# Optimization experiments

Hardware: AMD Instinct MI355X
Metric: run time of the kernel (lower is better)

The kernel has to match this reference:

```python
import jax, jax.numpy as jnp
import numpy as np

BINS = 6
THRESH = 0.2
OUT_HW = (240, 240)


def _normalize(x, lo=0.0, hi=1.0):
    # torch: if max-min==0 return zeros, else affine rescale to [lo, hi]
    mn, mx = x.min(), x.max()
    rng = mx - mn
    safe = jnp.where(rng == 0, 1.0, rng)
    out = (x - mn) / safe * (hi - lo) + lo
    return jnp.where(rng == 0, jnp.zeros_like(x), out)


def _ponder(x):
    w = (x.max() - x.mean()) ** 2
    return _normalize(x) * w


def _zero_border(x):
    # zero first/last row and column (works batched over leading dims)
    return (x.at[..., 0, :].set(0.0)
             .at[..., :, 0].set(0.0)
             .at[..., -1, :].set(0.0)
             .at[..., :, -1].set(0.0))


def _rarity(ch):
    # ch: [H, W] single feature channel
    ch = _zero_border(ch)
    ch = _normalize(ch, 0.0, 256.0)
    # torch.histc(bins=BINS, min=0, max=256): last bin includes the max value
    bin_idx = jnp.clip(jnp.floor(ch / (256.0 / BINS)), 0, BINS - 1).astype(jnp.int32)
    hist = jnp.zeros((BINS,), ch.dtype).at[bin_idx].add(1.0)
    hist = -jnp.log(hist / hist.sum() + 0.0001)
    # (channel * bins - 1).long().clamp(0, bins-1): .long() truncates toward zero
    gidx = jnp.clip(jnp.trunc(ch * BINS - 1.0), 0, BINS - 1).astype(jnp.int32)
    dst = _normalize(hist[gidx], 0.0, 1.0)
    return _ponder(dst)


def _apply_rarity(layer):
    # layer: [1, C, H, W] -> per-channel rarity, ponderated sum, threshold
    ch = layer[0]  # [C, H, W]
    r = jax.vmap(_rarity)(ch)  # [C, H, W]
    rz = _zero_border(r)
    # channel 0 keeps its border (torch code only zeroes borders for i >= 1)
    maps = jnp.concatenate([r[:1], rz[1:]], axis=0)
    proc = jax.vmap(_ponder)(maps).sum(0)
    proc = _normalize(proc, 0.0, 1.0)
    return jnp.where(proc < THRESH, 0.0, proc)


def _group(layer):
    resized = jax.image.resize(_apply_rarity(layer), OUT_HW, 'bilinear')
    # pack of one layer: fuse_itti == map_ponderation of the single map
    return _normalize(_ponder(resized), 0.0, 256.0)


def _forward(l1, l2, l3, l4, l5):
    groups = jnp.stack([_group(l) for l in (l1, l2, l3, l4, l5)], axis=-1)  # [240,240,5]
    return groups.sum(-1), groups


def setup_inputs() -> dict:
    key = jax.random.key(0)
    ks = jax.random.split(key, 5)
    shapes = [(1, 64, 480, 480), (1, 128, 240, 240), (1, 256, 120, 120),
              (1, 512, 60, 60), (1, 512, 30, 30)]
    return {f"l{i+1}": jax.random.uniform(ks[i], shapes[i], jnp.float32)
            for i in range(5)}


def reference(l1, l2, l3, l4, l5):
    return _forward(l1, l2, l3, l4, l5)
```

## Files before the change

### kernel.cpp

```cpp
#include <hip/hip_runtime.h>
#include <math.h>

#define TPB 256

constexpr int DIMS_[5]  = {480, 240, 120, 60, 30};
constexpr int CHS_ [5]  = {64, 128, 256, 512, 512};
constexpr int CHB_ [5]  = {0, 64, 192, 448, 960};
constexpr int TOTCH     = 1472;
constexpr int PROCB_[5] = {0, 230400, 288000, 302400, 306000};
constexpr int PROCTOT   = 306900;

constexpr int O_CHMIN = 0;
constexpr int O_CHMAX = 1472;
constexpr int O_HIST  = 2944;
constexpr int O_GCNT  = 11776;
constexpr int O_CLUT  = 20608;
constexpr int O_BSUM  = O_CLUT + 16 * 1472;
constexpr int O_PMIN  = O_BSUM + 5;
constexpr int O_PMAX  = O_PMIN + 5;
constexpr int O_S3MIN = O_PMAX + 5;
constexpr int O_S3MAX = O_S3MIN + 5;
constexpr int O_S3SUM = O_S3MAX + 5;
constexpr int O_PROC  = 44192;
constexpr int O_RESZ  = O_PROC + PROCTOT;
constexpr int N_INIT  = O_PROC + PROCTOT;

struct P {
  const float* in[5];
  float* ws;
};

__device__ __forceinline__ void mk_hthr(float mn, float rng, float* th) {
  if (rng == 0.0f) { th[0]=th[1]=th[2]=th[3]=th[4]=INFINITY; return; }
  th[0] = mn + rng * (1.0f / 6.0f); th[1] = mn + rng * (2.0f / 6.0f);
  th[2] = mn + rng * (3.0f / 6.0f); th[3] = mn + rng * (4.0f / 6.0f);
  th[4] = mn + rng * (5.0f / 6.0f);
}
__device__ __forceinline__ void mk_gthr(float mn, float rng, float* tg) {
  if (rng == 0.0f) { tg[0]=tg[1]=tg[2]=tg[3]=tg[4]=INFINITY; return; }
  tg[0] = mn + rng * (2.0f / 1536.0f); tg[1] = mn + rng * (3.0f / 1536.0f);
  tg[2] = mn + rng * (4.0f / 1536.0f); tg[3] = mn + rng * (5.0f / 1536.0f);
  tg[4] = mn + rng * (6.0f / 1536.0f);
}

__global__ void k_init(float* ws) {
  int i = blockIdx.x * TPB + threadIdx.x;
  if (i >= N_INIT) return;
  unsigned v = 0u;
  if (i < O_CHMAX) v = 0x7F800000u;
  else if (i >= O_PMIN  && i < O_PMAX)  v = 0x7F800000u;
  else if (i >= O_S3MIN && i < O_S3MAX) v = 0x7F800000u;
  ((unsigned*)ws)[i] = v;
}

template <int L>
__device__ void bodyA(int local, const float* __restrict__ in, float* ws) {
  constexpr int D = DIMS_[L], HW = D * D, HW4 = HW / 4;
  constexpr int BPC = (HW4 + 4095) / 4096;
  constexpr int DQ = D / 4;
  int ch = local / BPC, chunk = local % BPC;
  int nvec = HW4 - chunk * 4096; if (nvec > 4096) nvec = 4096;
  const float4* pv = (const float4*)(in + (size_t)ch * HW) + (size_t)chunk * 4096;
  int t = threadIdx.x;
  float mn = INFINITY, mx = 0.0f;
  #pragma unroll 4
  for (int i = 0; i < 16; i++) {
    int vi = i * TPB + t;
    if (vi < nvec) {
      float4 v = pv[vi];
      float vv[4] = {v.x, v.y, v.z, v.w};
      int f4i = chunk * 4096 + vi;
      if constexpr (D % 4 == 0) {
        int y = f4i / DQ, xq = f4i - y * DQ;
        if (y == 0 || y == D - 1) { vv[0] = vv[1] = vv[2] = vv[3] = 0.0f; }
        else {
          if (xq == 0)      vv[0] = 0.0f;
          if (xq == DQ - 1) vv[3] = 0.0f;
        }
      } else {
        int e0 = f4i * 4;
        #pragma unroll
        for (int j = 0; j < 4; j++) {
          int e = e0 + j, y = e / D, x = e - y * D;
          bool inr = ((unsigned)(x - 1) < (unsigned)(D - 2)) && ((unsigned)(y - 1) < (unsigned)(D - 2));
          if (!inr) vv[j] = 0.0f;
        }
      }
      #pragma unroll
      for (int j = 0; j < 4; j++) { mn = fminf(mn, vv[j]); mx = fmaxf(mx, vv[j]); }
    }
  }
  for (int o = 32; o; o >>= 1) { mn = fminf(mn, __shfl_down(mn, o)); mx = fmaxf(mx, __shfl_down(mx, o)); }
  __shared__ float smn[4], smx[4];
  int w = t >> 6;
  if ((t & 63) == 0) { smn[w] = mn; smx[w] = mx; }
  __syncthreads();
  if (t == 0) {
    mn = fminf(fminf(smn[0], smn[1]), fminf(smn[2], smn[3]));
    mx = fmaxf(fmaxf(smx[0], smx[1]), fmaxf(smx[2], smx[3]));
    int g = CHB_[L] + ch;
    atomicMin((unsigned*)ws + O_CHMIN + g, __float_as_uint(mn));
    atomicMax((unsigned*)ws + O_CHMAX + g, __float_as_uint(mx));
  }
}
__global__ void kA(P p) {
  int b = blockIdx.x;
  if      (b <  960) bodyA<0>(b,        p.in[0], p.ws);
  else if (b < 1472) bodyA<1>(b -  960, p.in[1], p.ws);
  else if (b < 1728) bodyA<2>(b - 1472, p.in[2], p.ws);
  else if (b < 2240) bodyA<3>(b - 1728, p.in[3], p.ws);
  else               bodyA<4>(b - 2240, p.in[4], p.ws);
}

template <int L>
__device__ void bodyB(int local, const float* __restrict__ in, float* ws) {
  constexpr int D = DIMS_[L], HW = D * D, HW4 = HW / 4;
  constexpr int BPC = (HW4 + 4095) / 4096;
  constexpr int DQ = D / 4;
  int ch = local / BPC, chunk = local % BPC;
  int g = CHB_[L] + ch;
  float mn = ws[O_CHMIN + g], mx = ws[O_CHMAX + g], rng = mx - mn;
  float th[5], tg[5];
  mk_hthr(mn, rng, th);
  mk_gthr(mn, rng, tg);
  int nvec = HW4 - chunk * 4096; if (nvec > 4096) nvec = 4096;
  const float4* pv = (const float4*)(in + (size_t)ch * HW) + (size_t)chunk * 4096;
  int t = threadIdx.x;
  unsigned c[10] = {0u,0u,0u,0u,0u,0u,0u,0u,0u,0u};
  unsigned nval = 0u;
  #pragma unroll 4
  for (int i = 0; i < 16; i++) {
    int vi = i * TPB + t;
    if (vi < nvec) {
      float4 v = pv[vi];
      float vv[4] = {v.x, v.y, v.z, v.w};
      int f4i = chunk * 4096 + vi;
      if constexpr (D % 4 == 0) {
        int y = f4i / DQ, xq = f4i - y * DQ;
        if (y == 0 || y == D - 1) { vv[0] = vv[1] = vv[2] = vv[3] = 0.0f; }
        else {
          if (xq == 0)      vv[0] = 0.0f;
          if (xq == DQ - 1) vv[3] = 0.0f;
        }
      } else {
        int e0 = f4i * 4;
        #pragma unroll
        for (int j = 0; j < 4; j++) {
          int e = e0 + j, y = e / D, x = e - y * D;
          bool inr = ((unsigned)(x - 1) < (unsigned)(D - 2)) && ((unsigned)(y - 1) < (unsigned)(D - 2));
          if (!inr) vv[j] = 0.0f;
        }
      }
      nval += 4u;
      #pragma unroll
      for (int j = 0; j < 4; j++) {
        float x = vv[j];
        #pragma unroll
        for (int k = 0; k < 5; k++) {
          c[k]     += (x >= th[k]);
          c[5 + k] += (x >= tg[k]);
        }
      }
    }
  }
  #pragma unroll
  for (int k = 0; k < 10; k++)
    for (int o = 32; o; o >>= 1) c[k] += __shfl_down(c[k], o);
  for (int o = 32; o; o >>= 1) nval += __shfl_down(nval, o);
  if ((t & 63) == 0) {
    unsigned* H = (unsigned*)ws + O_HIST + g * 6;
    unsigned* G = (unsigned*)ws + O_GCNT + g * 6;
    atomicAdd(H + 0, nval - c[0]); atomicAdd(H + 1, c[0] - c[1]);
    atomicAdd(H + 2, c[1] - c[2]); atomicAdd(H + 3, c[2] - c[3]);
    atomicAdd(H + 4, c[3] - c[4]); atomicAdd(H + 5, c[4]);
    atomicAdd(G + 0, nval - c[5]); atomicAdd(G + 1, c[5] - c[6]);
    atomicAdd(G + 2, c[6] - c[7]); atomicAdd(G + 3, c[7] - c[8]);
    atomicAdd(G + 4, c[8] - c[9]); atomicAdd(G + 5, c[9]);
  }
}
__global__ void kB(P p) {
  int b = blockIdx.x;
  if      (b <  960) bodyB<0>(b,        p.in[0], p.ws);
  else if (b < 1472) bodyB<1>(b -  960, p.in[1], p.ws);
  else if (b < 1728) bodyB<2>(b - 1472, p.in[2], p.ws);
  else if (b < 2240) bodyB<3>(b - 1728, p.in[3], p.ws);
  else               bodyB<4>(b - 2240, p.in[4], p.ws);
}

__global__ void kS(P p) {
  int ch = blockIdx.x * TPB + threadIdx.x;
  if (ch >= TOTCH) return;
  float* ws = p.ws;
  int l = (ch < 64) ? 0 : (ch < 192) ? 1 : (ch < 448) ? 2 : (ch < 960) ? 3 : 4;
  int D = DIMS_[l];
  int HW = D * D;
  int c0 = ch - CHB_[l];
  unsigned hc[6], gc[6];
  unsigned* H = (unsigned*)ws + O_HIST + ch * 6;
  unsigned* G = (unsigned*)ws + O_GCNT + ch * 6;
  #pragma unroll
  for (int k = 0; k < 6; k++) { hc[k] = H[k]; gc[k] = G[k]; }
  float HWf = (float)HW;
  float nh[6];
  #pragma unroll
  for (int k = 0; k < 6; k++) nh[k] = -logf((float)hc[k] / HWf + 1e-4f);
  float dmn = INFINITY, dmx = -INFINITY;
  #pragma unroll
  for (int k = 0; k < 6; k++) if (gc[k]) { dmn = fminf(dmn, nh[k]); dmx = fmaxf(dmx, nh[k]); }
  float dr = dmx - dmn;
  float dstn[6];
  #pragma unroll
  for (int k = 0; k < 6; k++) dstn[k] = (dr == 0.0f) ? 0.0f : ((nh[k] - dmn) / dr);
  float maxv = (dr == 0.0f) ? 0.0f : 1.0f;
  double s1 = 0.0;
  #pragma unroll
  for (int k = 0; k < 6; k++) s1 += (double)gc[k] * (double)dstn[k];
  float mean1 = (float)(s1 / (double)HW);
  float w1 = maxv - mean1; w1 *= w1;
  float lut1[6];
  #pragma unroll
  for (int k = 0; k < 6; k++) lut1[k] = dstn[k] * w1;
  float mnc = ws[O_CHMIN + ch], mxc = ws[O_CHMAX + ch];
  float tg[5];
  mk_gthr(mnc, mxc - mnc, tg);
  int gb = (0.0f >= tg[0]) + (0.0f >= tg[1]) + (0.0f >= tg[2]) + (0.0f >= tg[3]) + (0.0f >= tg[4]);
  unsigned bcnt = (unsigned)(4 * D - 4);
  float lmn, lmx;
  double s2 = 0.0;
  if (c0 == 0) {
    lmn = INFINITY; lmx = -INFINITY;
    #pragma unroll
    for (int k = 0; k < 6; k++) if (gc[k]) {
      lmn = fminf(lmn, lut1[k]); lmx = fmaxf(lmx, lut1[k]);
      s2 += (double)gc[k] * (double)lut1[k];
    }
  } else {
    lmn = 0.0f; lmx = 0.0f;
    #pragma unroll
    for (int k = 0; k < 6; k++) {
      unsigned ic = gc[k] - ((k == gb) ? bcnt : 0u);
      if (ic) {
        lmn = fminf(lmn, lut1[k]); lmx = fmaxf(lmx, lut1[k]);
        s2 += (double)ic * (double)lut1[k];
      }
    }
  }
  float mean2 = (float)(s2 / (double)HW);
  float w2 = lmx - mean2; w2 *= w2;
  float r2 = lmx - lmn;
  float lout[6];
  #pragma unroll
  for (int k = 0; k < 6; k++) lout[k] = (r2 == 0.0f) ? 0.0f : (((lut1[k] - lmn) / r2) * w2);
  float* T = ws + O_CLUT + (size_t)ch * 16;
  #pragma unroll
  for (int k = 0; k < 5; k++) T[5 + k] = tg[k];
  #pragma unroll
  for (int k = 0; k < 6; k++) T[10 + k] = lout[k];
  float bc = (c0 == 0) ? lout[gb] : ((r2 == 0.0f) ? 0.0f : (((0.0f - lmn) / r2) * w2));
  atomicAdd(ws + O_BSUM + l, bc);
}

template <int L>
__device__ void bodyC(int local, const float* __restrict__ in, float* ws,
                      float* slut, float* sred) {
  constexpr int D = DIMS_[L], HW = D * D, HW4 = HW / 4, C = CHS_[L];
  constexpr int NT  = (HW4 + 63) / 64;
  constexpr int NCH = C / 64;
  int tile = local % NT, chunk = local / NT;
  int cbase = CHB_[L] + chunk * 64;
  int t = threadIdx.x, lane = t & 63, w = t >> 6;
  const float* gl = ws + O_CLUT + (size_t)cbase * 16;
  for (int i = t; i < 1024; i += TPB) slut[i] = gl[i];
  __syncthreads();
  int p4 = tile * 64 + lane;
  bool valid = p4 < HW4;
  float a0 = 0.0f, a1 = 0.0f, a2 = 0.0f, a3 = 0.0f;
  if (valid) {
    const float4* bp = (const float4*)in + (size_t)(chunk * 64 + w * 16) * HW4 + p4;
    const float* su = slut + (w * 16) * 16;
    #pragma unroll 4
    for (int c = 0; c < 16; c++) {
      float4 v = bp[(size_t)c * HW4];
      const float* cl = su + c * 16 + 5;
      float g0 = cl[0], g1 = cl[1], g2 = cl[2], g3 = cl[3], g4 = cl[4];
      float l0 = cl[5], l1 = cl[6], l2 = cl[7], l3 = cl[8], l4 = cl[9], l5 = cl[10];
      float s;
      s = (v.x >= g0) ? l1 : l0; s = (v.x >= g1) ? l2 : s; s = (v.x >= g2) ? l3 : s;
      s = (v.x >= g3) ? l4 : s;  s = (v.x >= g4) ? l5 : s; a0 += s;
      s = (v.y >= g0) ? l1 : l0; s = (v.y >= g1) ? l2 : s; s = (v.y >= g2) ? l3 : s;
      s = (v.y >= g3) ? l4 : s;  s = (v.y >= g4) ? l5 : s; a1 += s;
      s = (v.z >= g0) ? l1 : l0; s = (v.z >= g1) ? l2 : s; s = (v.z >= g2) ? l3 : s;
      s = (v.z >= g3) ? l4 : s;  s = (v.z >= g4) ? l5 : s; a2 += s;
      s = (v.w >= g0) ? l1 : l0; s = (v.w >= g1) ? l2 : s; s = (v.w >= g2) ? l3 : s;
      s = (v.w >= g3) ? l4 : s;  s = (v.w >= g4) ? l5 : s; a3 += s;
    }
  }
  sred[0 * 256 + w * 64 + lane] = a0;
  sred[1 * 256 + w * 64 + lane] = a1;
  sred[2 * 256 + w * 64 + lane] = a2;
  sred[3 * 256 + w * 64 + lane] = a3;
  __syncthreads();
  if (w == 0 && valid) {
    float o[4];
    #pragma unroll
    for (int j = 0; j < 4; j++)
      o[j] = sred[j * 256 + lane] + sred[j * 256 + 64 + lane] +
             sred[j * 256 + 128 + lane] + sred[j * 256 + 192 + lane];
    float bs = ws[O_BSUM + L];
    float* procL = ws + O_PROC + PROCB_[L];
    int px0 = p4 * 4;
    if constexpr (NCH == 1) {
      #pragma unroll
      for (int j = 0; j < 4; j++) {
        int px = px0 + j, y = px / D, x = px - y * D;
        bool inr = ((unsigned)(x - 1) < (unsigned)(D - 2)) && ((unsigned)(y - 1) < (unsigned)(D - 2));
        if (!inr) o[j] = bs;
      }
      ((float4*)procL)[p4] = make_float4(o[0], o[1], o[2], o[3]);
    } else {
      #pragma unroll
      for (int j = 0; j < 4; j++) {
        int px = px0 + j, y = px / D, x = px - y * D;
        bool inr = ((unsigned)(x - 1) < (unsigned)(D - 2)) && ((unsigned)(y - 1) < (unsigned)(D - 2));
        if (inr) atomicAdd(procL + px, o[j]);
        else if (chunk == 0) procL[px] = bs;
      }
    }
  }
}
__global__ __launch_bounds__(TPB) void kC(P p) {
  __shared__ float slut[1024];
  __shared__ float sred[1024];
  int b = blockIdx.x;
  if      (b <  900) bodyC<0>(b,        p.in[0], p.ws, slut, sred);
  else if (b < 1350) bodyC<1>(b -  900, p.in[1], p.ws, slut, sred);
  else if (b < 1578) bodyC<2>(b - 1350, p.in[2], p.ws, slut, sred);
  else if (b < 1698) bodyC<3>(b - 1578, p.in[3], p.ws, slut, sred);
  else               bodyC<4>(b - 1698, p.in[4], p.ws, slut, sred);
}

template <int L>
__device__ void bodyD(int chunk, float* ws) {
  constexpr int HW = DIMS_[L] * DIMS_[L];
  const float* pr = ws + O_PROC + PROCB_[L];
  int t = threadIdx.x;
  float mn = INFINITY, mx = 0.0f;
  #pragma unroll
  for (int i = 0; i < 16; i++) {
    int idx = chunk * 4096 + i * TPB + t;
    if (idx < HW) { float v = pr[idx]; mn = fminf(mn, v); mx = fmaxf(mx, v); }
  }
  for (int o = 32; o; o >>= 1) { mn = fminf(mn, __shfl_down(mn, o)); mx = fmaxf(mx, __shfl_down(mx, o)); }
  __shared__ float smn[4], smx[4];
  int w = t >> 6;
  if ((t & 63) == 0) { smn[w] = mn; smx[w] = mx; }
  __syncthreads();
  if (t == 0) {
    mn = fminf(fminf(smn[0], smn[1]), fminf(smn[2], smn[3]));
    mx = fmaxf(fmaxf(smx[0], smx[1]), fmaxf(smx[2], smx[3]));
    atomicMin((unsigned*)ws + O_PMIN + L, __float_as_uint(mn));
    atomicMax((unsigned*)ws + O_PMAX + L, __float_as_uint(mx));
  }
}
__global__ void kD(P p) {
  int b = blockIdx.x;
  if      (b < 57) bodyD<0>(b,      p.ws);
  else if (b < 72) bodyD<1>(b - 57, p.ws);
  else if (b < 76) bodyD<2>(b - 72, p.ws);
  else if (b < 77) bodyD<3>(b - 76, p.ws);
  else             bodyD<4>(b - 77, p.ws);
}

template <int L>
__device__ float bodyF(int px, float* ws) {
  constexpr int D = DIMS_[L];
  constexpr float INV = (float)D / 240.0f;
  constexpr float KS = (INV > 1.0f) ? INV : 1.0f;
  int oy = px / 240, ox = px - oy * 240;
  float mnv = __uint_as_float(((unsigned*)ws)[O_PMIN + L]);
  float mxv = __uint_as_float(((unsigned*)ws)[O_PMAX + L]);
  float pr = mxv - mnv;
  const float* procL = ws + O_PROC + PROCB_[L];
  float sfy = ((float)oy + 0.5f) * INV - 0.5f;
  float sfx = ((float)ox + 0.5f) * INV - 0.5f;
  int y0 = (int)ceilf(sfy - KS);  if (y0 < 0) y0 = 0;
  int y1 = (int)floorf(sfy + KS); if (y1 > D - 1) y1 = D - 1;
  int x0 = (int)ceilf(sfx - KS);  if (x0 < 0) x0 = 0;
  int x1 = (int)floorf(sfx + KS); if (x1 > D - 1) x1 = D - 1;
  float wsx = 0.0f;
  for (int jx = x0; jx <= x1; jx++) wsx += fmaxf(1.0f - fabsf(sfx - (float)jx) / KS, 0.0f);
  float acc = 0.0f, wsy = 0.0f;
  for (int jy = y0; jy <= y1; jy++) {
    float wy = fmaxf(1.0f - fabsf(sfy - (float)jy) / KS, 0.0f);
    wsy += wy;
    if (wy > 0.0f) {
      const float* row = procL + jy * D;
      float rs = 0.0f;
      for (int jx = x0; jx <= x1; jx++) {
        float wx = fmaxf(1.0f - fabsf(sfx - (float)jx) / KS, 0.0f);
        if (wx > 0.0f) {
          float v = row[jx];
          float tv = (pr == 0.0f) ? 0.0f : ((v - mnv) / pr);
          tv = (tv < 0.2f) ? 0.0f : tv;
          rs += wx * tv;
        }
      }
      acc += wy * rs;
    }
  }
  return acc / (wsy * wsx);
}
__global__ void kF(P p) {
  float* ws = p.ws;
  int b = blockIdx.x, l = b / 225;
  int px = (b - l * 225) * TPB + threadIdx.x;
  float res;
  switch (l) {
    case 0: res = bodyF<0>(px, ws); break;
    case 1: res = bodyF<1>(px, ws); break;
    case 2: res = bodyF<2>(px, ws); break;
    case 3: res = bodyF<3>(px, ws); break;
    default: res = bodyF<4>(px, ws); break;
  }
  ws[O_RESZ + l * 57600 + px] = res;
  float mn = res, mx = res, s = res;
  for (int o = 32; o; o >>= 1) {
    mn = fminf(mn, __shfl_down(mn, o));
    mx = fmaxf(mx, __shfl_down(mx, o));
    s += __shfl_down(s, o);
  }
  __shared__ float smn[4], smx[4], ssm[4];
  int t = threadIdx.x, w = t >> 6;
  if ((t & 63) == 0) { smn[w] = mn; smx[w] = mx; ssm[w] = s; }
  __syncthreads();
  if (t == 0) {
    mn = fminf(fminf(smn[0], smn[1]), fminf(smn[2], smn[3]));
    mx = fmaxf(fmaxf(smx[0], smx[1]), fmaxf(smx[2], smx[3]));
    s = ssm[0] + ssm[1] + ssm[2] + ssm[3];
    atomicMin((unsigned*)ws + O_S3MIN + l, __float_as_uint(mn));
    atomicMax((unsigned*)ws + O_S3MAX + l, __float_as_uint(mx));
    atomicAdd(ws + O_S3SUM + l, s);
  }
}

__global__ void kG2(P p, float* __restrict__ out) {
  float* ws = p.ws;
  int px = blockIdx.x * TPB + threadIdx.x;
  float sum = 0.0f;
  #pragma unroll
  for (int l = 0; l < 5; l++) {
    float v = ws[O_RESZ + l * 57600 + px];
    float mn3 = __uint_as_float(((unsigned*)ws)[O_S3MIN + l]);
    float mx3 = __uint_as_float(((unsigned*)ws)[O_S3MAX + l]);
    float mean3 = ws[O_S3SUM + l] / 57600.0f;
    float r3 = mx3 - mn3;
    float ov;
    if (r3 == 0.0f) ov = 0.0f;
    else {
      float w3 = mx3 - mean3; w3 *= w3;
      if (w3 == 0.0f) ov = 0.0f;
      else ov = ((v - mn3) / r3) * w3 / w3 * 256.0f;
    }
    out[57600 + px * 5 + l] = ov;
    sum += ov;
  }
  out[px] = sum;
}

extern "C" void kernel_launch(void* const* d_in, const int* in_sizes, int n_in,
                              void* d_out, int out_size, void* d_ws, size_t ws_size,
                              hipStream_t stream) {
  (void)in_sizes; (void)n_in; (void)out_size; (void)ws_size;
  P p;
  for (int i = 0; i < 5; i++) p.in[i] = (const float*)d_in[i];
  p.ws = (float*)d_ws;
  float* out = (float*)d_out;

  k_init<<<(N_INIT + TPB - 1) / TPB, TPB, 0, stream>>>(p.ws);
  kA  <<<2752, TPB, 0, stream>>>(p);
  kB  <<<2752, TPB, 0, stream>>>(p);
  kS  <<<6,    TPB, 0, stream>>>(p);
  kC  <<<1730, TPB, 0, stream>>>(p);
  kD  <<<78,   TPB, 0, stream>>>(p);
  kF  <<<1125, TPB, 0, stream>>>(p);
  kG2 <<<225,  TPB, 0, stream>>>(p, out);
}
```

Before: 288.6 us.

## Software-pipeline loads in reduction kernels and move border masking out of histogram pass

The min/max, histogram and LUT-accumulate loops now use explicit double-buffered float4 loads in groups of four, so the next group's global loads are issued before the current group is processed. The histogram pass no longer zeroes border pixels per element. Extra blocks instead subtract the border pixels' raw counts, and the summary kernel adds back the border count as zeros. Per-thread nval tracking is dropped and the LUT layout in workspace is reindexed. This trades extra blocks, atomics and register pressure for less index arithmetic and better latency hiding in the bandwidth-bound passes.

```diff
diff --git a/kernel.cpp b/kernel.cpp
--- a/kernel.cpp
+++ b/kernel.cpp
@@ -53,6 +53,16 @@
   ((unsigned*)ws)[i] = v;
 }
 
+template <int D, int DQ>
+__device__ __forceinline__ void zb4(int f4i, float4& v) {
+  int y = f4i / DQ, xq = f4i - y * DQ;
+  if (y == 0 || y == D - 1) { v.x = v.y = v.z = v.w = 0.0f; }
+  else {
+    if (xq == 0)      v.x = 0.0f;
+    if (xq == DQ - 1) v.w = 0.0f;
+  }
+}
+
 template <int L>
 __device__ void bodyA(int local, const float* __restrict__ in, float* ws) {
   constexpr int D = DIMS_[L], HW = D * D, HW4 = HW / 4;
@@ -63,31 +73,56 @@
   const float4* pv = (const float4*)(in + (size_t)ch * HW) + (size_t)chunk * 4096;
   int t = threadIdx.x;
   float mn = INFINITY, mx = 0.0f;
-  #pragma unroll 4
-  for (int i = 0; i < 16; i++) {
-    int vi = i * TPB + t;
-    if (vi < nvec) {
-      float4 v = pv[vi];
-      float vv[4] = {v.x, v.y, v.z, v.w};
-      int f4i = chunk * 4096 + vi;
-      if constexpr (D % 4 == 0) {
-        int y = f4i / DQ, xq = f4i - y * DQ;
-        if (y == 0 || y == D - 1) { vv[0] = vv[1] = vv[2] = vv[3] = 0.0f; }
-        else {
-          if (xq == 0)      vv[0] = 0.0f;
-          if (xq == DQ - 1) vv[3] = 0.0f;
+  auto MM4 = [&](float4 v) {
+    mn = fminf(fminf(mn, fminf(v.x, v.y)), fminf(v.z, v.w));
+    mx = fmaxf(fmaxf(mx, fmaxf(v.x, v.y)), fmaxf(v.z, v.w));
+  };
+  if constexpr (D % 4 == 0) {
+    if (nvec == 4096) {
+      int base = chunk * 4096;
+      float4 a0 = pv[t], a1 = pv[t + TPB], a2 = pv[t + 2 * TPB], a3 = pv[t + 3 * TPB];
+      #pragma unroll
+      for (int g = 0; g < 4; g++) {
+        float4 b0 = a0, b1 = a1, b2 = a2, b3 = a3;
+        if (g < 3) {
+          int o = (g + 1) * 4 * TPB + t;
+          b0 = pv[o]; b1 = pv[o + TPB]; b2 = pv[o + 2 * TPB]; b3 = pv[o + 3 * TPB];
         }
-      } else {
-        int e0 = f4i * 4;
+        int i0 = base + g * 4 * TPB + t;
+        zb4<D, DQ>(i0,           a0); MM4(a0);
+        zb4<D, DQ>(i0 + TPB,     a1); MM4(a1);
+        zb4<D, DQ>(i0 + 2 * TPB, a2); MM4(a2);
+        zb4<D, DQ>(i0 + 3 * TPB, a3); MM4(a3);
+        a0 = b0; a1 = b1; a2 = b2; a3 = b3;
+      }
+    } else {
+      #pragma unroll 4
+      for (int i = 0; i < 16; i++) {
+        int vi = i * TPB + t;
+        if (vi < nvec) {
+          float4 v = pv[vi];
+          zb4<D, DQ>(chunk * 4096 + vi, v);
+          MM4(v);
+        }
+      }
+    }
+  } else {
+    #pragma unroll 4
+    for (int i = 0; i < 16; i++) {
+      int vi = i * TPB + t;
+      if (vi < nvec) {
+        float4 v = pv[vi];
+        float vv[4] = {v.x, v.y, v.z, v.w};
+        int e0 = (chunk * 4096 + vi) * 4;
         #pragma unroll
         for (int j = 0; j < 4; j++) {
           int e = e0 + j, y = e / D, x = e - y * D;
           bool inr = ((unsigned)(x - 1) < (unsigned)(D - 2)) && ((unsigned)(y - 1) < (unsigned)(D - 2));
           if (!inr) vv[j] = 0.0f;
         }
-      }
-      #pragma unroll
-      for (int j = 0; j < 4; j++) { mn = fminf(mn, vv[j]); mx = fmaxf(mx, vv[j]); }
+        v.x = vv[0]; v.y = vv[1]; v.z = vv[2]; v.w = vv[3];
+        MM4(v);
+      }
     }
   }
   for (int o = 32; o; o >>= 1) { mn = fminf(mn, __shfl_down(mn, o)); mx = fmaxf(mx, __shfl_down(mx, o)); }
@@ -116,7 +151,6 @@
 __device__ void bodyB(int local, const float* __restrict__ in, float* ws) {
   constexpr int D = DIMS_[L], HW = D * D, HW4 = HW / 4;
   constexpr int BPC = (HW4 + 4095) / 4096;
-  constexpr int DQ = D / 4;
   int ch = local / BPC, chunk = local % BPC;
   int g = CHB_[L] + ch;
   float mn = ws[O_CHMIN + g], mx = ws[O_CHMAX + g], rng = mx - mn;
@@ -127,59 +161,79 @@
   const float4* pv = (const float4*)(in + (size_t)ch * HW) + (size_t)chunk * 4096;
   int t = threadIdx.x;
   unsigned c[10] = {0u,0u,0u,0u,0u,0u,0u,0u,0u,0u};
-  unsigned nval = 0u;
-  #pragma unroll 4
-  for (int i = 0; i < 16; i++) {
-    int vi = i * TPB + t;
-    if (vi < nvec) {
-      float4 v = pv[vi];
-      float vv[4] = {v.x, v.y, v.z, v.w};
-      int f4i = chunk * 4096 + vi;
-      if constexpr (D % 4 == 0) {
-        int y = f4i / DQ, xq = f4i - y * DQ;
-        if (y == 0 || y == D - 1) { vv[0] = vv[1] = vv[2] = vv[3] = 0.0f; }
-        else {
-          if (xq == 0)      vv[0] = 0.0f;
-          if (xq == DQ - 1) vv[3] = 0.0f;
-        }
-      } else {
-        int e0 = f4i * 4;
-        #pragma unroll
-        for (int j = 0; j < 4; j++) {
-          int e = e0 + j, y = e / D, x = e - y * D;
-          bool inr = ((unsigned)(x - 1) < (unsigned)(D - 2)) && ((unsigned)(y - 1) < (unsigned)(D - 2));
-          if (!inr) vv[j] = 0.0f;
-        }
-      }
-      nval += 4u;
-      #pragma unroll
-      for (int j = 0; j < 4; j++) {
-        float x = vv[j];
-        #pragma unroll
-        for (int k = 0; k < 5; k++) {
-          c[k]     += (x >= th[k]);
-          c[5 + k] += (x >= tg[k]);
-        }
-      }
+  auto CNT = [&](float x) {
+    #pragma unroll
+    for (int k = 0; k < 5; k++) { c[k] += (x >= th[k]); c[5 + k] += (x >= tg[k]); }
+  };
+  auto CNT4 = [&](float4 v) { CNT(v.x); CNT(v.y); CNT(v.z); CNT(v.w); };
+  if (nvec == 4096) {
+    float4 a0 = pv[t], a1 = pv[t + TPB], a2 = pv[t + 2 * TPB], a3 = pv[t + 3 * TPB];
+    #pragma unroll
+    for (int gq = 0; gq < 4; gq++) {
+      float4 b0 = a0, b1 = a1, b2 = a2, b3 = a3;
+      if (gq < 3) {
+        int o = (gq + 1) * 4 * TPB + t;
+        b0 = pv[o]; b1 = pv[o + TPB]; b2 = pv[o + 2 * TPB]; b3 = pv[o + 3 * TPB];
+      }
+      CNT4(a0); CNT4(a1); CNT4(a2); CNT4(a3);
+      a0 = b0; a1 = b1; a2 = b2; a3 = b3;
+    }
+  } else {
+    #pragma unroll 4
+    for (int i = 0; i < 16; i++) {
+      int vi = i * TPB + t;
+      if (vi < nvec) CNT4(pv[vi]);
     }
   }
   #pragma unroll
   for (int k = 0; k < 10; k++)
     for (int o = 32; o; o >>= 1) c[k] += __shfl_down(c[k], o);
-  for (int o = 32; o; o >>= 1) nval += __shfl_down(nval, o);
   if ((t & 63) == 0) {
     unsigned* H = (unsigned*)ws + O_HIST + g * 6;
     unsigned* G = (unsigned*)ws + O_GCNT + g * 6;
-    atomicAdd(H + 0, nval - c[0]); atomicAdd(H + 1, c[0] - c[1]);
-    atomicAdd(H + 2, c[1] - c[2]); atomicAdd(H + 3, c[2] - c[3]);
-    atomicAdd(H + 4, c[3] - c[4]); atomicAdd(H + 5, c[4]);
-    atomicAdd(G + 0, nval - c[5]); atomicAdd(G + 1, c[5] - c[6]);
-    atomicAdd(G + 2, c[6] - c[7]); atomicAdd(G + 3, c[7] - c[8]);
-    atomicAdd(G + 4, c[8] - c[9]); atomicAdd(G + 5, c[9]);
-  }
-}
+    #pragma unroll
+    for (int k = 0; k < 5; k++) { atomicAdd(H + k, c[k]); atomicAdd(G + k, c[5 + k]); }
+  }
+}
+
+__device__ void bodyBborder(int ch, P p) {
+  float* ws = p.ws;
+  int l = (ch < 64) ? 0 : (ch < 192) ? 1 : (ch < 448) ? 2 : (ch < 960) ? 3 : 4;
+  int D = DIMS_[l];
+  const float* src = p.in[l] + (size_t)(ch - CHB_[l]) * (D * D);
+  float mn = ws[O_CHMIN + ch], mx = ws[O_CHMAX + ch], rng = mx - mn;
+  float th[5], tg[5];
+  mk_hthr(mn, rng, th);
+  mk_gthr(mn, rng, tg);
+  unsigned c[10] = {0u,0u,0u,0u,0u,0u,0u,0u,0u,0u};
+  int nb = 4 * D - 4;
+  for (int e = threadIdx.x; e < nb; e += TPB) {
+    int x, y;
+    if (e < D)          { y = 0; x = e; }
+    else if (e < 2 * D) { y = D - 1; x = e - D; }
+    else {
+      int e2 = e - 2 * D;
+      y = 1 + (e2 >> 1);
+      x = (e2 & 1) ? (D - 1) : 0;
+    }
+    float v = src[y * D + x];
+    #pragma unroll
+    for (int k = 0; k < 5; k++) { c[k] += (v >= th[k]); c[5 + k] += (v >= tg[k]); }
+  }
+  #pragma unroll
+  for (int k = 0; k < 10; k++)
+    for (int o = 32; o; o >>= 1) c[k] += __shfl_down(c[k], o);
+  if ((threadIdx.x & 63) == 0) {
+    unsigned* H = (unsigned*)ws + O_HIST + ch * 6;
+    unsigned* G = (unsigned*)ws + O_GCNT + ch * 6;
+    #pragma unroll
+    for (int k = 0; k < 5; k++) { atomicSub(H + k, c[k]); atomicSub(G + k, c[5 + k]); }
+  }
+}
+
 __global__ void kB(P p) {
   int b = blockIdx.x;
+  if (b >= 2752) { bodyBborder(b - 2752, p); return; }
   if      (b <  960) bodyB<0>(b,        p.in[0], p.ws);
   else if (b < 1472) bodyB<1>(b -  960, p.in[1], p.ws);
   else if (b < 1728) bodyB<2>(b - 1472, p.in[2], p.ws);
@@ -195,11 +249,27 @@
   int D = DIMS_[l];
   int HW = D * D;
   int c0 = ch - CHB_[l];
-  unsigned hc[6], gc[6];
   unsigned* H = (unsigned*)ws + O_HIST + ch * 6;
   unsigned* G = (unsigned*)ws + O_GCNT + ch * 6;
-  #pragma unroll
-  for (int k = 0; k < 6; k++) { hc[k] = H[k]; gc[k] = G[k]; }
+  unsigned cH[5], cG[5];
+  #pragma unroll
+  for (int k = 0; k < 5; k++) { cH[k] = H[k]; cG[k] = G[k]; }
+  float mnc = ws[O_CHMIN + ch], mxc = ws[O_CHMAX + ch];
+  float thh[5], tg[5];
+  mk_hthr(mnc, mxc - mnc, thh);
+  mk_gthr(mnc, mxc - mnc, tg);
+  unsigned bcnt = (unsigned)(4 * D - 4);
+  unsigned czH[5], czG[5];
+  #pragma unroll
+  for (int k = 0; k < 5; k++) {
+    czH[k] = cH[k] + bcnt * (unsigned)(0.0f >= thh[k]);
+    czG[k] = cG[k] + bcnt * (unsigned)(0.0f >= tg[k]);
+  }
+  unsigned hc[6], gc[6];
+  hc[0] = (unsigned)HW - czH[0]; hc[5] = czH[4];
+  gc[0] = (unsigned)HW - czG[0]; gc[5] = czG[4];
+  #pragma unroll
+  for (int k = 1; k < 5; k++) { hc[k] = czH[k - 1] - czH[k]; gc[k] = czG[k - 1] - czG[k]; }
   float HWf = (float)HW;
   float nh[6];
   #pragma unroll
@@ -220,11 +290,7 @@
   float lut1[6];
   #pragma unroll
   for (int k = 0; k < 6; k++) lut1[k] = dstn[k] * w1;
-  float mnc = ws[O_CHMIN + ch], mxc = ws[O_CHMAX + ch];
-  float tg[5];
-  mk_gthr(mnc, mxc - mnc, tg);
   int gb = (0.0f >= tg[0]) + (0.0f >= tg[1]) + (0.0f >= tg[2]) + (0.0f >= tg[3]) + (0.0f >= tg[4]);
-  unsigned bcnt = (unsigned)(4 * D - 4);
   float lmn, lmx;
   double s2 = 0.0;
   if (c0 == 0) {
@@ -253,9 +319,9 @@
   for (int k = 0; k < 6; k++) lout[k] = (r2 == 0.0f) ? 0.0f : (((lut1[k] - lmn) / r2) * w2);
   float* T = ws + O_CLUT + (size_t)ch * 16;
   #pragma unroll
-  for (int k = 0; k < 5; k++) T[5 + k] = tg[k];
-  #pragma unroll
-  for (int k = 0; k < 6; k++) T[10 + k] = lout[k];
+  for (int k = 0; k < 5; k++) T[k] = tg[k];
+  #pragma unroll
+  for (int k = 0; k < 6; k++) T[8 + k] = lout[k];
   float bc = (c0 == 0) ? lout[gb] : ((r2 == 0.0f) ? 0.0f : (((0.0f - lmn) / r2) * w2));
   atomicAdd(ws + O_BSUM + l, bc);
 }
@@ -278,12 +344,10 @@
   if (valid) {
     const float4* bp = (const float4*)in + (size_t)(chunk * 64 + w * 16) * HW4 + p4;
     const float* su = slut + (w * 16) * 16;
-    #pragma unroll 4
-    for (int c = 0; c < 16; c++) {
-      float4 v = bp[(size_t)c * HW4];
-      const float* cl = su + c * 16 + 5;
+    auto PROC = [&](float4 v, int c) {
+      const float* cl = su + c * 16;
       float g0 = cl[0], g1 = cl[1], g2 = cl[2], g3 = cl[3], g4 = cl[4];
-      float l0 = cl[5], l1 = cl[6], l2 = cl[7], l3 = cl[8], l4 = cl[9], l5 = cl[10];
+      float l0 = cl[8], l1 = cl[9], l2 = cl[10], l3 = cl[11], l4 = cl[12], l5 = cl[13];
       float s;
       s = (v.x >= g0) ? l1 : l0; s = (v.x >= g1) ? l2 : s; s = (v.x >= g2) ? l3 : s;
       s = (v.x >= g3) ? l4 : s;  s = (v.x >= g4) ? l5 : s; a0 += s;
@@ -293,6 +357,18 @@
       s = (v.z >= g3) ? l4 : s;  s = (v.z >= g4) ? l5 : s; a2 += s;
       s = (v.w >= g0) ? l1 : l0; s = (v.w >= g1) ? l2 : s; s = (v.w >= g2) ? l3 : s;
       s = (v.w >= g3) ? l4 : s;  s = (v.w >= g4) ? l5 : s; a3 += s;
+    };
+    float4 va0 = bp[0], va1 = bp[(size_t)HW4], va2 = bp[(size_t)2 * HW4], va3 = bp[(size_t)3 * HW4];
+    #pragma unroll
+    for (int gq = 0; gq < 4; gq++) {
+      float4 vb0 = va0, vb1 = va1, vb2 = va2, vb3 = va3;
+      if (gq < 3) {
+        const float4* np = bp + (size_t)(gq + 1) * 4 * HW4;
+        vb0 = np[0]; vb1 = np[(size_t)HW4]; vb2 = np[(size_t)2 * HW4]; vb3 = np[(size_t)3 * HW4];
+      }
+      PROC(va0, gq * 4 + 0); PROC(va1, gq * 4 + 1);
+      PROC(va2, gq * 4 + 2); PROC(va3, gq * 4 + 3);
+      va0 = vb0; va1 = vb1; va2 = vb2; va3 = vb3;
     }
   }
   sred[0 * 256 + w * 64 + lane] = a0;
@@ -478,7 +554,7 @@
 
   k_init<<<(N_INIT + TPB - 1) / TPB, TPB, 0, stream>>>(p.ws);
   kA  <<<2752, TPB, 0, stream>>>(p);
-  kB  <<<2752, TPB, 0, stream>>>(p);
+  kB  <<<2752 + TOTCH, TPB, 0, stream>>>(p);
   kS  <<<6,    TPB, 0, stream>>>(p);
   kC  <<<1730, TPB, 0, stream>>>(p);
   kD  <<<78,   TPB, 0, stream>>>(p);
```

After: 305.7 us. 1.06x slower.
